# Kernel tuning notes

Hardware: AMD Instinct MI355X
Metric: run time of the kernel (lower is better)

The kernel has to match this reference:

```python
import jax, jax.numpy as jnp
import numpy as np

D_MODEL = 1024
NUM_EXPERTS = 16
TOP_K = 2
TOP_C = 4  # min(M, max(4, 2*K))
RANK = 64  # max(4, d_model // 16) per choose_lowrank_r
TAU = 1.0


def setup_inputs() -> dict:
    key = jax.random.key(0)
    ks = jax.random.split(key, 7)
    B = 32768
    x = jax.random.normal(ks[0], (B, D_MODEL), dtype=jnp.float32)
    # shared encoder Linear(d, d) with bias
    We = jax.random.normal(ks[1], (D_MODEL, D_MODEL), dtype=jnp.float32) / np.sqrt(D_MODEL)
    be = jnp.zeros((D_MODEL,), dtype=jnp.float32)
    # gating Linear(d, M), no bias
    Wg = jax.random.normal(ks[2], (NUM_EXPERTS, D_MODEL), dtype=jnp.float32) / np.sqrt(D_MODEL)
    # per-expert LoRA weights: U: [M, r, d], V: [M, d, r], gamma: [M]
    U = jax.random.normal(ks[3], (NUM_EXPERTS, RANK, D_MODEL), dtype=jnp.float32) / np.sqrt(D_MODEL)
    V = jax.random.normal(ks[4], (NUM_EXPERTS, D_MODEL, RANK), dtype=jnp.float32) / np.sqrt(RANK)
    gamma = jnp.ones((NUM_EXPERTS,), dtype=jnp.float32)
    return {"x": x, "We": We, "be": be, "Wg": Wg, "U": U, "V": V, "gamma": gamma}


def reference(x, We, be, Wg, U, V, gamma):
    B = x.shape[0]
    encoded = x @ We.T + be                       # [B, d]
    logits = (encoded @ Wg.T) / TAU               # [B, M]
    # Top-C candidate selection, then Top-K among candidates
    topc_vals, topc_idx = jax.lax.top_k(logits, TOP_C)          # [B, C]
    topk_vals, pos_in_c = jax.lax.top_k(topc_vals, TOP_K)       # [B, K]
    topk_idx = jnp.take_along_axis(topc_idx, pos_in_c, axis=1)  # [B, K]
    # masked stable softmax over selected logits (matches _stable_masked_softmax)
    e = jnp.exp(topk_vals - jnp.max(topk_vals, axis=1, keepdims=True))
    w = e / (jnp.sum(e, axis=1, keepdims=True) + 1e-12)
    w = jnp.where(w > 1e-12, w, 0.0)  # keep_mask: drop negligible weights
    # scatter routing weights into dense [B, M] combine matrix
    w_full = jnp.zeros((B, NUM_EXPERTS), x.dtype).at[
        jnp.arange(B)[:, None], topk_idx].add(w)
    # expert residual delta: E(x) = x + gamma * V @ silu(U @ x)
    hidden = jax.nn.silu(jnp.einsum('bd,mrd->bmr', encoded, U))  # [B, M, r]
    delta = jnp.einsum('bmr,mdr,bm->bd', hidden, V, w_full * gamma[None, :])
    # y = encoded + sum_k w_k * (E_k(encoded) - encoded); sum_k w_k = 1
    return encoded + delta
```

## Files before the change

kernel.cpp:

```cpp
#include <hip/hip_runtime.h>
#include <stdint.h>

#define B_TOK 32768
#define DM 1024
#define NEXP 16
#define RK 64
#define NPAIR 256
#define TPT 64
#define HT 128
#define GRID_CMB 3072
#define GRID_HID 544
#define MAXTILE 1024

typedef unsigned short u16;
typedef __bf16 bf16x8 __attribute__((ext_vector_type(8)));
typedef float f32x4 __attribute__((ext_vector_type(4)));

__device__ __forceinline__ u16 f2bf(float f) {
  union { float f; uint32_t u; } v; v.f = f;
  return (u16)((v.u + 0x7fffu + ((v.u >> 16) & 1u)) >> 16);
}
__device__ __forceinline__ float bf2f(u16 u) {
  union { uint32_t i; float f; } v; v.i = ((uint32_t)u) << 16; return v.f;
}

__device__ __forceinline__ void gload_lds16(const void* g, void* l) {
  __builtin_amdgcn_global_load_lds(
      (const __attribute__((address_space(1))) void*)g,
      (__attribute__((address_space(3))) void*)l, 16, 0, 0);
}

__global__ void k_convert3(const float* __restrict__ s0, u16* __restrict__ d0,
                           const float* __restrict__ s1, u16* __restrict__ d1,
                           const float* __restrict__ s2, u16* __restrict__ d2) {
  const int seg = blockIdx.x >> 8;
  const int bid = blockIdx.x & 255;
  const float* src = (seg == 0) ? s0 : (seg == 1) ? s1 : s2;
  u16* dst = (seg == 0) ? d0 : (seg == 1) ? d1 : d2;
  int i = bid * 256 + threadIdx.x;
  #pragma unroll
  for (int v = 0; v < 4; ++v) {
    int idx = i + v * 65536;
    float4 f = reinterpret_cast<const float4*>(src)[idx];
    ushort4 o;
    o.x = f2bf(f.x); o.y = f2bf(f.y); o.z = f2bf(f.z); o.w = f2bf(f.w);
    reinterpret_cast<ushort4*>(dst)[idx] = o;
  }
}

__global__ void k_wgeff(const float* __restrict__ Wg, const float* __restrict__ We,
                        const float* __restrict__ be,
                        float* __restrict__ Wgeff, float* __restrict__ gbias) {
  int e = blockIdx.y;
  int d = blockIdx.x * 256 + threadIdx.x;
  double acc = 0.0;
  for (int k = 0; k < DM; ++k)
    acc += (double)Wg[e * DM + k] * (double)We[k * DM + d];
  Wgeff[e * DM + d] = (float)acc;
  if (blockIdx.x == 0 && threadIdx.x == 0) {
    double s = 0.0;
    for (int k = 0; k < DM; ++k) s += (double)be[k] * (double)Wg[e * DM + k];
    gbias[e] = (float)s;
  }
}

#define GT 64
#define GD 128

__global__ __launch_bounds__(256) void k_gating(
    const float* __restrict__ x, u16* __restrict__ x_bf,
    const float* __restrict__ Wgeff, const float* __restrict__ gbias,
    const float* __restrict__ gamma,
    int* __restrict__ tk_pid, float* __restrict__ tk_w0, float* __restrict__ tk_w1,
    int* __restrict__ counts_p, int* __restrict__ counts_e) {
  __shared__ float xs[GT][GD + 4];
  __shared__ float wsd[NEXP][GD + 4];
  __shared__ float lg[GT][NEXP + 2];
  __shared__ int bcnt[NPAIR];
  __shared__ int bexp[NEXP];
  const int tid = threadIdx.x;
  const int tok0 = blockIdx.x * GT;
  const int t0 = (tid >> 3) * 2;
  const int e0 = (tid & 7) * 2;
  bcnt[tid] = 0;
  if (tid < NEXP) bexp[tid] = 0;

  double acc00 = 0.0, acc01 = 0.0, acc10 = 0.0, acc11 = 0.0;

  for (int c = 0; c < DM; c += GD) {
    __syncthreads();
    #pragma unroll
    for (int v = 0; v < (GT * GD / 4) / 256; ++v) {
      int idx = tid + v * 256;
      int r = idx >> 5, cc = idx & 31;
      float4 v4 = *reinterpret_cast<const float4*>(x + (size_t)(tok0 + r) * DM + c + cc * 4);
      *reinterpret_cast<float4*>(&xs[r][cc * 4]) = v4;
      ushort4 o;
      o.x = f2bf(v4.x); o.y = f2bf(v4.y); o.z = f2bf(v4.z); o.w = f2bf(v4.w);
      *reinterpret_cast<ushort4*>(x_bf + (size_t)(tok0 + r) * DM + c + cc * 4) = o;
    }
    #pragma unroll
    for (int v = 0; v < (NEXP * GD / 4) / 256; ++v) {
      int idx = tid + v * 256;
      int r = idx >> 5, cc = idx & 31;
      *reinterpret_cast<float4*>(&wsd[r][cc * 4]) =
          *reinterpret_cast<const float4*>(Wgeff + (size_t)r * DM + c + cc * 4);
    }
    __syncthreads();
    #pragma unroll 8
    for (int d = 0; d < GD; d += 4) {
      float4 xa = *reinterpret_cast<const float4*>(&xs[t0][d]);
      float4 xb = *reinterpret_cast<const float4*>(&xs[t0 + 1][d]);
      float4 wa = *reinterpret_cast<const float4*>(&wsd[e0][d]);
      float4 wb = *reinterpret_cast<const float4*>(&wsd[e0 + 1][d]);
      acc00 += (double)xa.x * wa.x + (double)xa.y * wa.y + (double)xa.z * wa.z + (double)xa.w * wa.w;
      acc01 += (double)xa.x * wb.x + (double)xa.y * wb.y + (double)xa.z * wb.z + (double)xa.w * wb.w;
      acc10 += (double)xb.x * wa.x + (double)xb.y * wa.y + (double)xb.z * wa.z + (double)xb.w * wa.w;
      acc11 += (double)xb.x * wb.x + (double)xb.y * wb.y + (double)xb.z * wb.z + (double)xb.w * wb.w;
    }
  }

  lg[t0][e0]         = (float)(acc00 + (double)gbias[e0]);
  lg[t0][e0 + 1]     = (float)(acc01 + (double)gbias[e0 + 1]);
  lg[t0 + 1][e0]     = (float)(acc10 + (double)gbias[e0]);
  lg[t0 + 1][e0 + 1] = (float)(acc11 + (double)gbias[e0 + 1]);
  __syncthreads();

  if (tid < GT) {
    int tok = tok0 + tid;
    float v0 = lg[tid][0]; int i0 = 0;
    #pragma unroll
    for (int j = 1; j < NEXP; ++j)
      if (lg[tid][j] > v0) { v0 = lg[tid][j]; i0 = j; }
    float v1 = -3.4e38f; int i1 = 0;
    #pragma unroll
    for (int j = 0; j < NEXP; ++j) {
      if (j == i0) continue;
      if (lg[tid][j] > v1) { v1 = lg[tid][j]; i1 = j; }
    }
    float e1 = expf(v1 - v0);
    float denom = 1.0f + e1 + 1e-12f;
    float w0 = 1.0f / denom, w1 = e1 / denom;
    if (!(w0 > 1e-12f)) w0 = 0.0f;
    if (!(w1 > 1e-12f)) w1 = 0.0f;
    int pid = i0 * 16 + i1;
    tk_pid[tok] = pid;
    tk_w0[tok] = w0 * gamma[i0];
    tk_w1[tok] = w1 * gamma[i1];
    atomicAdd(&bcnt[pid], 1);
    atomicAdd(&bexp[i0], 1);
    atomicAdd(&bexp[i1], 1);
  }
  __syncthreads();
  if (bcnt[tid] > 0) atomicAdd(&counts_p[tid], bcnt[tid]);
  if (tid < NEXP && bexp[tid] > 0) atomicAdd(&counts_e[tid], bexp[tid]);
}

__global__ __launch_bounds__(NPAIR) void k_scan(
    const int* __restrict__ counts_p, const int* __restrict__ counts_e,
    int* __restrict__ offs_p, int* __restrict__ curs_p,
    int* __restrict__ offs_e, int* __restrict__ curs_e,
    int* __restrict__ tp_pair, int* __restrict__ tp_loc, int* __restrict__ n_tp,
    int* __restrict__ th_exp, int* __restrict__ th_loc, int* __restrict__ n_th) {
  __shared__ int sc[NPAIR], st[NPAIR];
  __shared__ int seb[NEXP + 1], thb[NEXP + 1];
  const int tid = threadIdx.x;
  const int c = counts_p[tid];
  const int nt = (c + TPT - 1) / TPT;
  sc[tid] = c; st[tid] = nt;
  __syncthreads();
  for (int s = 1; s < NPAIR; s <<= 1) {
    int vc = 0, vt = 0;
    if (tid >= s) { vc = sc[tid - s]; vt = st[tid - s]; }
    __syncthreads();
    sc[tid] += vc; st[tid] += vt;
    __syncthreads();
  }
  const int offc = sc[tid] - c;
  const int offt = st[tid] - nt;
  offs_p[tid] = offc;
  curs_p[tid] = offc;
  if (tid == NPAIR - 1) { offs_p[NPAIR] = sc[tid]; n_tp[0] = st[tid]; }
  for (int q = 0; q < nt; ++q) { tp_pair[offt + q] = tid; tp_loc[offt + q] = q * TPT; }

  if (tid == 0) {
    int s = 0, s2 = 0;
    for (int e = 0; e < NEXP; ++e) {
      seb[e] = s; thb[e] = s2;
      int ce = counts_e[e];
      s += ce; s2 += (ce + HT - 1) / HT;
    }
    seb[NEXP] = s; thb[NEXP] = s2;
    n_th[0] = s2;
  }
  __syncthreads();
  if (tid <= NEXP) offs_e[tid] = seb[tid];
  if (tid < NEXP) {
    curs_e[tid] = seb[tid];
    int ce = counts_e[tid];
    int ntt = (ce + HT - 1) / HT;
    for (int q = 0; q < ntt; ++q) { th_exp[thb[tid] + q] = tid; th_loc[thb[tid] + q] = q * HT; }
  }
}

__global__ __launch_bounds__(256) void k_scatter(
    const int* __restrict__ tk_pid, const float* __restrict__ tk_w0,
    const float* __restrict__ tk_w1,
    int* __restrict__ curs_p, int* __restrict__ curs_e,
    int* __restrict__ a_tok, int* __restrict__ a_h0,
    int* __restrict__ a_h1,
    int* __restrict__ e_tok, float* __restrict__ e_w) {
  __shared__ int hp[NPAIR];
  __shared__ int he[NEXP];
  __shared__ int bp[NPAIR];
  __shared__ int beB[NEXP];
  const int tid = threadIdx.x;
  const int tok = blockIdx.x * 256 + tid;
  hp[tid] = 0;
  if (tid < NEXP) he[tid] = 0;
  __syncthreads();

  const int pid = tk_pid[tok];
  const int i0 = pid >> 4, i1 = pid & 15;
  const int rp = atomicAdd(&hp[pid], 1);
  const int r0 = atomicAdd(&he[i0], 1);
  const int r1 = atomicAdd(&he[i1], 1);
  __syncthreads();

  if (hp[tid] > 0) bp[tid] = atomicAdd(&curs_p[tid], hp[tid]);
  if (tid < NEXP && he[tid] > 0) beB[tid] = atomicAdd(&curs_e[tid], he[tid]);
  __syncthreads();

  const int posp = bp[pid] + rp;
  const int pos0 = beB[i0] + r0;
  const int pos1 = beB[i1] + r1;
  a_tok[posp] = tok;
  a_h0[posp] = pos0;
  a_h1[posp] = pos1;
  e_tok[pos0] = tok; e_w[pos0] = tk_w0[tok];
  e_tok[pos1] = tok; e_w[pos1] = tk_w1[tok];
}

__global__ __launch_bounds__(256) void k_encoder(
    const u16* __restrict__ A, const u16* __restrict__ Bm,
    const float* __restrict__ bias, u16* __restrict__ Cb) {
  __shared__ __align__(16) u16 As[128 * 64];
  __shared__ __align__(16) u16 Bs[128 * 64];
  const int nwg = gridDim.x * gridDim.y;
  const int orig = blockIdx.y * gridDim.x + blockIdx.x;
  const int qq = nwg >> 3;
  const int swz = (orig & 7) * qq + (orig >> 3);
  const int m0 = (swz / gridDim.x) * 128, n0 = (swz % gridDim.x) * 128;
  const int tid = threadIdx.x;
  const int lane = tid & 63, wave = tid >> 6;
  const int wr = wave >> 1, wc = wave & 1;
  const int lrow = lane & 15, lhi = lane >> 4;

  f32x4 acc[4][4];
  #pragma unroll
  for (int i = 0; i < 4; ++i)
    #pragma unroll
    for (int j = 0; j < 4; ++j) acc[i][j] = (f32x4){0.f, 0.f, 0.f, 0.f};

  const u16* gA0; const u16* gA1; const u16* gA2; const u16* gA3;
  const u16* gB0; const u16* gB1; const u16* gB2; const u16* gB3;
  int dOf0, dOf1, dOf2, dOf3;
  {
    int slot, row, c, sc;
    slot = tid;         row = slot >> 3; c = slot & 7; sc = (c ^ (row & 7)) * 8;
    gA0 = A + (size_t)(m0 + row) * DM + sc; gB0 = Bm + (size_t)(n0 + row) * DM + sc; dOf0 = slot * 8;
    slot = tid + 256;   row = slot >> 3; c = slot & 7; sc = (c ^ (row & 7)) * 8;
    gA1 = A + (size_t)(m0 + row) * DM + sc; gB1 = Bm + (size_t)(n0 + row) * DM + sc; dOf1 = slot * 8;
    slot = tid + 512;   row = slot >> 3; c = slot & 7; sc = (c ^ (row & 7)) * 8;
    gA2 = A + (size_t)(m0 + row) * DM + sc; gB2 = Bm + (size_t)(n0 + row) * DM + sc; dOf2 = slot * 8;
    slot = tid + 768;   row = slot >> 3; c = slot & 7; sc = (c ^ (row & 7)) * 8;
    gA3 = A + (size_t)(m0 + row) * DM + sc; gB3 = Bm + (size_t)(n0 + row) * DM + sc; dOf3 = slot * 8;
  }

  const int rk0 = ((0 + lhi) ^ (lrow & 7)) * 8;
  const int rk1 = ((4 + lhi) ^ (lrow & 7)) * 8;

  for (int k0 = 0; k0 < DM; k0 += 64) {
    __syncthreads();
    gload_lds16(gA0 + k0, As + dOf0);
    gload_lds16(gA1 + k0, As + dOf1);
    gload_lds16(gA2 + k0, As + dOf2);
    gload_lds16(gA3 + k0, As + dOf3);
    gload_lds16(gB0 + k0, Bs + dOf0);
    gload_lds16(gB1 + k0, Bs + dOf1);
    gload_lds16(gB2 + k0, Bs + dOf2);
    gload_lds16(gB3 + k0, Bs + dOf3);
    __syncthreads();
    #pragma unroll
    for (int kk = 0; kk < 2; ++kk) {
      const int rk = kk ? rk1 : rk0;
      bf16x8 a[4], b[4];
      #pragma unroll
      for (int mi = 0; mi < 4; ++mi)
        a[mi] = *reinterpret_cast<const bf16x8*>(&As[(wr * 64 + mi * 16 + lrow) * 64 + rk]);
      #pragma unroll
      for (int nj = 0; nj < 4; ++nj)
        b[nj] = *reinterpret_cast<const bf16x8*>(&Bs[(wc * 64 + nj * 16 + lrow) * 64 + rk]);
      #pragma unroll
      for (int mi = 0; mi < 4; ++mi)
        #pragma unroll
        for (int nj = 0; nj < 4; ++nj)
          acc[mi][nj] = __builtin_amdgcn_mfma_f32_16x16x32_bf16(a[mi], b[nj], acc[mi][nj], 0, 0, 0);
    }
  }

  const int orow = lhi * 4, ocol = lrow;
  #pragma unroll
  for (int mi = 0; mi < 4; ++mi) {
    #pragma unroll
    for (int nj = 0; nj < 4; ++nj) {
      int gcol = n0 + wc * 64 + nj * 16 + ocol;
      float bv = bias[gcol];
      #pragma unroll
      for (int r = 0; r < 4; ++r) {
        int grow = m0 + wr * 64 + mi * 16 + orow + r;
        Cb[(size_t)grow * DM + gcol] = f2bf(acc[mi][nj][r] + bv);
      }
    }
  }
}

__global__ __launch_bounds__(256) void k_hidden(
    const u16* __restrict__ Enc, const u16* __restrict__ Ub,
    const int* __restrict__ offs_e, const int* __restrict__ th_exp,
    const int* __restrict__ th_loc, const int* __restrict__ n_th,
    const int* __restrict__ e_tok, const float* __restrict__ e_w,
    u16* __restrict__ Hws) {
  const int bswz = (blockIdx.x & 7) * (GRID_HID >> 3) + (blockIdx.x >> 3);
  if (bswz >= n_th[0]) return;
  const int e = th_exp[bswz];
  const int loc0 = th_loc[bswz];
  const int base = offs_e[e];
  const int cnt = offs_e[e + 1] - base;
  const int tid = threadIdx.x;
  const int lane = tid & 63, wave = tid >> 6;
  const int lrow = lane & 15;
  const int lkb = (lane >> 4) * 16;

  __shared__ float s_ew[HT];
  __shared__ __align__(16) u16 Us[64 * 512];
  if (tid < HT) {
    int i = loc0 + tid;
    s_ew[tid] = (i < cnt) ? e_w[base + i] : 0.0f;
  }

  const u16* aP[2];
  #pragma unroll
  for (int mi = 0; mi < 2; ++mi) {
    int ridx = loc0 + wave * 32 + mi * 16 + lrow;
    int v = ridx < cnt;
    int tok = e_tok[base + (v ? ridx : 0)];
    aP[mi] = Enc + (size_t)tok * DM + (lane >> 4) * 8;
  }

  f32x4 acc[2][4];
  #pragma unroll
  for (int i = 0; i < 2; ++i)
    #pragma unroll
    for (int j = 0; j < 4; ++j) acc[i][j] = (f32x4){0.f, 0.f, 0.f, 0.f};

  const char* Ue = (const char*)(Ub + (size_t)e * RK * DM);

  for (int half = 0; half < 2; ++half) {
    __syncthreads();
    #pragma unroll
    for (int it = 0; it < 16; ++it) {
      int D = (tid + it * 256) * 16;
      int row = D >> 10, bo = D & 1023;
      int sbo = bo ^ ((row & 7) << 4);
      gload_lds16(Ue + (size_t)row * 2048 + half * 1024 + sbo, ((char*)Us) + D);
    }
    __syncthreads();
    #pragma unroll 4
    for (int step = 0; step < 16; ++step) {
      const int k0 = half * 512 + step * 32;
      bf16x8 b[4];
      #pragma unroll
      for (int nj = 0; nj < 4; ++nj) {
        int n = nj * 16 + lrow;
        int bofs = n * 1024 + ((step * 64 + lkb) ^ ((n & 7) << 4));
        b[nj] = *reinterpret_cast<const bf16x8*>(((const char*)Us) + bofs);
      }
      bf16x8 a0 = *reinterpret_cast<const bf16x8*>(aP[0] + k0);
      bf16x8 a1 = *reinterpret_cast<const bf16x8*>(aP[1] + k0);
      #pragma unroll
      for (int nj = 0; nj < 4; ++nj) {
        acc[0][nj] = __builtin_amdgcn_mfma_f32_16x16x32_bf16(a0, b[nj], acc[0][nj], 0, 0, 0);
        acc[1][nj] = __builtin_amdgcn_mfma_f32_16x16x32_bf16(a1, b[nj], acc[1][nj], 0, 0, 0);
      }
    }
  }

  #pragma unroll
  for (int mi = 0; mi < 2; ++mi)
    #pragma unroll
    for (int nj = 0; nj < 4; ++nj)
      #pragma unroll
      for (int rr = 0; rr < 4; ++rr) {
        int rloc = wave * 32 + mi * 16 + (lane >> 4) * 4 + rr;
        if (loc0 + rloc < cnt) {
          float z = acc[mi][nj][rr];
          float h = z / (1.0f + expf(-z)) * s_ew[rloc];
          Hws[(size_t)(base + loc0 + rloc) * RK + nj * 16 + (lane & 15)] = f2bf(h);
        }
      }
}

__global__ __launch_bounds__(256) void k_combine(
    const u16* __restrict__ Enc, const u16* __restrict__ Vb,
    const u16* __restrict__ Hws, const int* __restrict__ offs_p,
    const int* __restrict__ tp_pair, const int* __restrict__ tp_loc,
    const int* __restrict__ n_tp, const int* __restrict__ a_tok,
    const int* __restrict__ a_h0, const int* __restrict__ a_h1,
    float* __restrict__ Out) {
  const int bswz = (blockIdx.x & 7) * (GRID_CMB >> 3) + (blockIdx.x >> 3);
  const int t = bswz >> 2;
  const int p = bswz & 3;
  if (t >= n_tp[0]) return;
  const int pid = tp_pair[t];
  const int pe0 = pid >> 4, pe1 = pid & 15;
  const int base = offs_p[pid];
  const int cnt = offs_p[pid + 1] - base;
  const int loc0 = tp_loc[t];
  const int tid = threadIdx.x;
  const int lane = tid & 63, wave = tid >> 6;

  __shared__ int s_tok[TPT];
  __shared__ int s_h0[TPT];
  __shared__ int s_h1[TPT];
  __shared__ int s_val[TPT];
  if (tid < TPT) {
    int idx = loc0 + tid;
    int v = idx < cnt;
    int pp = base + (v ? idx : 0);
    s_val[tid] = v;
    s_tok[tid] = a_tok[pp];
    s_h0[tid] = a_h0[pp];
    s_h1[tid] = a_h1[pp];
  }
  __syncthreads();

  const int lrow = lane & 15, lk = (lane >> 4) * 8;
  const int col0 = p * 256 + wave * 64;

  bf16x8 hb[4][4];
  #pragma unroll
  for (int kk = 0; kk < 4; ++kk)
    #pragma unroll
    for (int tf = 0; tf < 4; ++tf) {
      int tok = tf * 16 + lrow;
      int hidx = (kk < 2) ? s_h0[tok] : s_h1[tok];
      hb[kk][tf] = *reinterpret_cast<const bf16x8*>(
          Hws + (size_t)hidx * RK + (kk & 1) * 32 + lk);
    }

  ushort4 encv[4][4];
  #pragma unroll
  for (int mi = 0; mi < 4; ++mi)
    #pragma unroll
    for (int tf = 0; tf < 4; ++tf) {
      int tok = tf * 16 + (lane & 15);
      int d = col0 + mi * 16 + (lane >> 4) * 4;
      encv[mi][tf] = *reinterpret_cast<const ushort4*>(Enc + (size_t)s_tok[tok] * DM + d);
    }

  const u16* V0 = Vb + (size_t)pe0 * DM * RK;
  const u16* V1 = Vb + (size_t)pe1 * DM * RK;

  f32x4 acc2[4][4];
  #pragma unroll
  for (int i = 0; i < 4; ++i)
    #pragma unroll
    for (int j = 0; j < 4; ++j) acc2[i][j] = (f32x4){0.f, 0.f, 0.f, 0.f};

  #pragma unroll
  for (int kk = 0; kk < 4; ++kk) {
    const u16* Vsel = (kk < 2) ? V0 : V1;
    const int kof = (kk & 1) * 32 + lk;
    #pragma unroll
    for (int mi = 0; mi < 4; ++mi) {
      int d = col0 + mi * 16 + lrow;
      bf16x8 va = *reinterpret_cast<const bf16x8*>(Vsel + (size_t)d * RK + kof);
      #pragma unroll
      for (int tf = 0; tf < 4; ++tf)
        acc2[mi][tf] = __builtin_amdgcn_mfma_f32_16x16x32_bf16(va, hb[kk][tf], acc2[mi][tf], 0, 0, 0);
    }
  }

  #pragma unroll
  for (int mi = 0; mi < 4; ++mi)
    #pragma unroll
    for (int tf = 0; tf < 4; ++tf) {
      int tok = tf * 16 + (lane & 15);
      if (!s_val[tok]) continue;
      int d = col0 + mi * 16 + (lane >> 4) * 4;
      size_t ro = (size_t)s_tok[tok] * DM + d;
      ushort4 ev = encv[mi][tf];
      float4 o;
      o.x = acc2[mi][tf][0] + bf2f(ev.x);
      o.y = acc2[mi][tf][1] + bf2f(ev.y);
      o.z = acc2[mi][tf][2] + bf2f(ev.z);
      o.w = acc2[mi][tf][3] + bf2f(ev.w);
      *reinterpret_cast<float4*>(Out + ro) = o;
    }
}

extern "C" void kernel_launch(void* const* d_in, const int* in_sizes, int n_in,
                              void* d_out, int out_size, void* d_ws, size_t ws_size,
                              hipStream_t stream) {
  const float* x = (const float*)d_in[0];
  const float* We = (const float*)d_in[1];
  const float* be = (const float*)d_in[2];
  const float* Wg = (const float*)d_in[3];
  const float* U = (const float*)d_in[4];
  const float* V = (const float*)d_in[5];
  const float* gamma = (const float*)d_in[6];
  float* Out = (float*)d_out;

  char* ws = (char*)d_ws;
  size_t off = 0;
  auto alloc = [&](size_t bytes) -> void* {
    void* p = ws + off;
    off += (bytes + 255) & ~(size_t)255;
    return p;
  };
  u16* x_bf   = (u16*)alloc((size_t)B_TOK * DM * 2);
  u16* enc_bf = (u16*)alloc((size_t)B_TOK * DM * 2);
  u16* We_bf  = (u16*)alloc((size_t)DM * DM * 2);
  u16* U_bf   = (u16*)alloc((size_t)NEXP * RK * DM * 2);
  u16* V_bf   = (u16*)alloc((size_t)NEXP * DM * RK * 2);
  u16* Hws    = (u16*)alloc(((size_t)2 * B_TOK + HT) * RK * 2);
  float* Wgeff = (float*)alloc((size_t)NEXP * DM * 4);
  float* gbias = (float*)alloc(NEXP * 4);
  int* tk_pid  = (int*)alloc((size_t)B_TOK * 4);
  float* tk_w0 = (float*)alloc((size_t)B_TOK * 4);
  float* tk_w1 = (float*)alloc((size_t)B_TOK * 4);
  int* counts_p = (int*)alloc(NPAIR * 4);
  int* counts_e = (int*)alloc(NEXP * 4);
  int* offs_p   = (int*)alloc((NPAIR + 1) * 4);
  int* curs_p   = (int*)alloc(NPAIR * 4);
  int* offs_e   = (int*)alloc((NEXP + 1) * 4);
  int* curs_e   = (int*)alloc(NEXP * 4);
  int* tp_pair  = (int*)alloc(MAXTILE * 4);
  int* tp_loc   = (int*)alloc(MAXTILE * 4);
  int* n_tp     = (int*)alloc(256);
  int* th_exp   = (int*)alloc(MAXTILE * 4);
  int* th_loc   = (int*)alloc(MAXTILE * 4);
  int* n_th     = (int*)alloc(256);
  int* a_tok   = (int*)alloc((size_t)B_TOK * 4);
  int* a_h0    = (int*)alloc((size_t)B_TOK * 4);
  int* a_h1    = (int*)alloc((size_t)B_TOK * 4);
  int* e_tok   = (int*)alloc(((size_t)2 * B_TOK + HT) * 4);
  float* e_w   = (float*)alloc(((size_t)2 * B_TOK + HT) * 4);
  (void)ws_size; (void)in_sizes; (void)n_in; (void)out_size;

  hipMemsetAsync(counts_p, 0, NPAIR * 4, stream);
  hipMemsetAsync(counts_e, 0, NEXP * 4, stream);

  k_convert3<<<768, 256, 0, stream>>>(We, We_bf, U, U_bf, V, V_bf);
  k_wgeff<<<dim3(4, 16), 256, 0, stream>>>(Wg, We, be, Wgeff, gbias);
  k_gating<<<B_TOK / GT, 256, 0, stream>>>(x, x_bf, Wgeff, gbias, gamma,
                                           tk_pid, tk_w0, tk_w1, counts_p, counts_e);
  k_scan<<<1, NPAIR, 0, stream>>>(counts_p, counts_e, offs_p, curs_p, offs_e, curs_e,
                                  tp_pair, tp_loc, n_tp, th_exp, th_loc, n_th);
  k_scatter<<<B_TOK / 256, 256, 0, stream>>>(tk_pid, tk_w0, tk_w1, curs_p, curs_e,
                                             a_tok, a_h0, a_h1, e_tok, e_w);
  k_encoder<<<dim3(DM / 128, B_TOK / 128), 256, 0, stream>>>(x_bf, We_bf, be, enc_bf);
  k_hidden<<<GRID_HID, 256, 0, stream>>>(enc_bf, U_bf, offs_e, th_exp, th_loc, n_th,
                                         e_tok, e_w, Hws);
  k_combine<<<GRID_CMB, 256, 0, stream>>>(enc_bf, V_bf, Hws, offs_p, tp_pair, tp_loc,
                                          n_tp, a_tok, a_h0, a_h1, Out);
}
```

Measured before the change: 366.4 us.

## Double-buffer encoder GEMM LDS tiles to overlap global loads with MFMA

Splits the encoder GEMM's shared-memory tiles into two ping-pong buffers. The next K-slice is issued as direct global-to-LDS loads while MFMAs run on the current slice, with vmcnt waits and barriers in place of full syncthreads. The aim is to hide global-load latency behind compute. In exchange, LDS use per block doubles to 64KB, which may lower occupancy. Correctness also depends on the hand-written vmcnt counts and on the LDS-direct loads being ordered correctly.

```diff
diff --git a/kernel.cpp b/kernel.cpp
--- a/kernel.cpp
+++ b/kernel.cpp
@@ -244,8 +244,10 @@
 __global__ __launch_bounds__(256) void k_encoder(
     const u16* __restrict__ A, const u16* __restrict__ Bm,
     const float* __restrict__ bias, u16* __restrict__ Cb) {
-  __shared__ __align__(16) u16 As[128 * 64];
-  __shared__ __align__(16) u16 Bs[128 * 64];
+  __shared__ __align__(16) u16 As0[128 * 64];
+  __shared__ __align__(16) u16 Bs0[128 * 64];
+  __shared__ __align__(16) u16 As1[128 * 64];
+  __shared__ __align__(16) u16 Bs1[128 * 64];
   const int nwg = gridDim.x * gridDim.y;
   const int orig = blockIdx.y * gridDim.x + blockIdx.x;
   const int qq = nwg >> 3;
@@ -280,33 +282,52 @@
   const int rk0 = ((0 + lhi) ^ (lrow & 7)) * 8;
   const int rk1 = ((4 + lhi) ^ (lrow & 7)) * 8;
 
-  for (int k0 = 0; k0 < DM; k0 += 64) {
-    __syncthreads();
-    gload_lds16(gA0 + k0, As + dOf0);
-    gload_lds16(gA1 + k0, As + dOf1);
-    gload_lds16(gA2 + k0, As + dOf2);
-    gload_lds16(gA3 + k0, As + dOf3);
-    gload_lds16(gB0 + k0, Bs + dOf0);
-    gload_lds16(gB1 + k0, Bs + dOf1);
-    gload_lds16(gB2 + k0, Bs + dOf2);
-    gload_lds16(gB3 + k0, Bs + dOf3);
-    __syncthreads();
+  auto STAGE = [&](u16* Ad, u16* Bd, int k0) {
+    gload_lds16(gA0 + k0, Ad + dOf0);
+    gload_lds16(gA1 + k0, Ad + dOf1);
+    gload_lds16(gA2 + k0, Ad + dOf2);
+    gload_lds16(gA3 + k0, Ad + dOf3);
+    gload_lds16(gB0 + k0, Bd + dOf0);
+    gload_lds16(gB1 + k0, Bd + dOf1);
+    gload_lds16(gB2 + k0, Bd + dOf2);
+    gload_lds16(gB3 + k0, Bd + dOf3);
+  };
+  auto COMPUTE = [&](const u16* Ar, const u16* Br) {
     #pragma unroll
     for (int kk = 0; kk < 2; ++kk) {
       const int rk = kk ? rk1 : rk0;
       bf16x8 a[4], b[4];
       #pragma unroll
       for (int mi = 0; mi < 4; ++mi)
-        a[mi] = *reinterpret_cast<const bf16x8*>(&As[(wr * 64 + mi * 16 + lrow) * 64 + rk]);
+        a[mi] = *reinterpret_cast<const bf16x8*>(&Ar[(wr * 64 + mi * 16 + lrow) * 64 + rk]);
       #pragma unroll
       for (int nj = 0; nj < 4; ++nj)
-        b[nj] = *reinterpret_cast<const bf16x8*>(&Bs[(wc * 64 + nj * 16 + lrow) * 64 + rk]);
+        b[nj] = *reinterpret_cast<const bf16x8*>(&Br[(wc * 64 + nj * 16 + lrow) * 64 + rk]);
       #pragma unroll
       for (int mi = 0; mi < 4; ++mi)
         #pragma unroll
         for (int nj = 0; nj < 4; ++nj)
           acc[mi][nj] = __builtin_amdgcn_mfma_f32_16x16x32_bf16(a[mi], b[nj], acc[mi][nj], 0, 0, 0);
     }
+  };
+
+  STAGE(As0, Bs0, 0);
+  #pragma unroll
+  for (int i = 0; i < 8; ++i) {
+    STAGE(As1, Bs1, i * 128 + 64);
+    asm volatile("s_waitcnt vmcnt(8)" ::: "memory");
+    __builtin_amdgcn_s_barrier();
+    COMPUTE(As0, Bs0);
+    __builtin_amdgcn_s_barrier();
+    if (i < 7) {
+      STAGE(As0, Bs0, i * 128 + 128);
+      asm volatile("s_waitcnt vmcnt(8)" ::: "memory");
+    } else {
+      asm volatile("s_waitcnt vmcnt(0)" ::: "memory");
+    }
+    __builtin_amdgcn_s_barrier();
+    COMPUTE(As1, Bs1);
+    __builtin_amdgcn_s_barrier();
   }
 
   const int orow = lhi * 4, ocol = lrow;
```

New measurement: 360.9 us. About the same (-1.5%).
